# Kernel optimization log

Measured on AMD Instinct MI355X. Metric: run time of the kernel, lower is better.

## Reference

```python
import jax, jax.numpy as jnp
from jax import lax
import numpy as np

SEQ, FEAT, VOCAB = 59, 64, 578
B, U = 4096, 1024


def setup_inputs() -> dict:
    key = jax.random.key(0)
    ks = jax.random.split(key, 6)
    x = jax.random.normal(ks[0], (B, SEQ, FEAT), dtype=jnp.float32)
    # Keras LSTMCell params: kernel [feat, 4U], recurrent_kernel [U, 4U], bias [4U]
    kernel = jax.random.normal(ks[1], (FEAT, 4 * U), dtype=jnp.float32) * 0.05
    rec_kernel = jax.random.normal(ks[2], (U, 4 * U), dtype=jnp.float32) * 0.05
    bias = jnp.zeros((4 * U,), dtype=jnp.float32)
    w2 = jax.random.normal(ks[3], (U, VOCAB), dtype=jnp.float32) * 0.05
    b2 = jnp.zeros((VOCAB,), dtype=jnp.float32)
    return {"x": x, "kernel": kernel, "rec_kernel": rec_kernel, "bias": bias, "w2": w2, "b2": b2}


def reference(x, kernel, rec_kernel, bias, w2, b2):
    batch = x.shape[0]
    units = rec_kernel.shape[0]
    xs = jnp.transpose(x, (1, 0, 2))  # [SEQ, B, FEAT]
    h0 = jnp.zeros((batch, units), dtype=x.dtype)
    c0 = jnp.zeros((batch, units), dtype=x.dtype)

    def step(carry, xt):
        h, c = carry
        z = xt @ kernel + h @ rec_kernel + bias  # [B, 4U]
        i, f, g, o = jnp.split(z, 4, axis=-1)    # Keras gate order i,f,c,o
        i = jax.nn.sigmoid(i)
        f = jax.nn.sigmoid(f)
        g = jnp.tanh(g)
        o = jax.nn.sigmoid(o)
        c_new = f * c + i * g
        h_new = o * jnp.tanh(c_new)
        return (h_new, c_new), None

    (h_last, _), _ = lax.scan(step, (h0, c0), xs)
    probs = jax.nn.softmax(h_last @ w2 + b2, axis=-1)  # dense2 softmax on last hidden
    # original: stack single prediction -> [1,B,V], transpose [1,0,2] -> [B,1,V]
    return probs[:, None, :]
```

## Files before the change

kernel.cpp:

```cpp
#include <hip/hip_runtime.h>

#define SEQ    59
#define FEAT   64
#define VOCAB  578
#define BATCH  4096
#define UNITS  1024
#define KLSTM  1088
#define NPAD   640

typedef __bf16 bf16x8 __attribute__((ext_vector_type(8)));
typedef __bf16 bf16x4 __attribute__((ext_vector_type(4)));
typedef float  floatx4 __attribute__((ext_vector_type(4)));

typedef const __attribute__((address_space(1))) char gas_char;
typedef __attribute__((address_space(3))) char las_char;

__device__ __forceinline__ float sigmoid_f(float x) { return 1.f / (1.f + __expf(-x)); }
__device__ __forceinline__ float tanh_f(float x) { float e = __expf(2.f * x); return 1.f - 2.f / (e + 1.f); }


__global__ void convert_x_kernel(const float* __restrict__ x, __bf16* __restrict__ xbf) {
    int i = blockIdx.x * 256 + threadIdx.x;
    const int total = BATCH * SEQ * FEAT / 4;
    if (i >= total) return;
    float4 v = ((const float4*)x)[i];
    bf16x4 o;
    o.x = (__bf16)v.x; o.y = (__bf16)v.y; o.z = (__bf16)v.z; o.w = (__bf16)v.w;
    ((bf16x4*)xbf)[i] = o;
}

__global__ void convert_weights_kernel(const float* __restrict__ kern,
                                       const float* __restrict__ reck,
                                       __bf16* __restrict__ Wtp) {
    int idx = blockIdx.x * 256 + threadIdx.x;
    if (idx >= 4096 * KLSTM) return;
    int np = idx / KLSTM;
    int k  = idx - np * KLSTM;
    int ublk = np >> 7;
    int g    = (np >> 5) & 3;
    int j    = np & 31;
    int n    = g * 1024 + ublk * 32 + j;
    float v = (k < FEAT) ? kern[(size_t)k * 4096 + n]
                         : reck[(size_t)(k - FEAT) * 4096 + n];
    Wtp[idx] = (__bf16)v;
}

__global__ void convert_w2_kernel(const float* __restrict__ w2, __bf16* __restrict__ Wt2p) {
    int idx = blockIdx.x * 256 + threadIdx.x;
    if (idx >= NPAD * 1024) return;
    int n = idx >> 10;
    int k = idx & 1023;
    float v = (n < VOCAB) ? w2[(size_t)k * VOCAB + n] : 0.f;
    Wt2p[idx] = (__bf16)v;
}

__global__ void __launch_bounds__(256, 2) lstm_step_kernel(
    const __bf16* __restrict__ xbf,
    const __bf16* __restrict__ Wtp,
    const float*  __restrict__ bias,
    const __bf16* __restrict__ hin,
    __bf16*       __restrict__ hout,
    float*        __restrict__ cstate,
    int t)
{
    __shared__ __bf16 As[128 * 64];
    __shared__ __bf16 Bs[2][128 * 64];

    const int tid  = threadIdx.x;
    const int wid  = tid >> 6;
    const int lane = tid & 63;
    const int ln   = lane & 15;
    const int lk   = lane >> 4;
    const int wm   = wid >> 1;
    const int wn   = wid & 1;
    const int rb   = blockIdx.x;
    const int yb   = blockIdx.y;

    floatx4 acc[2][4][4];
#pragma unroll
    for (int p = 0; p < 2; ++p)
#pragma unroll
        for (int m = 0; m < 4; ++m)
#pragma unroll
            for (int g = 0; g < 4; ++g)
                acc[p][m][g] = (floatx4){0.f, 0.f, 0.f, 0.f};

    int s_row[4], s_kgd[4];
#pragma unroll
    for (int q = 0; q < 4; ++q) {
        int flat = q * 256 + tid;
        int row  = flat >> 3;
        s_row[q] = row;
        s_kgd[q] = (flat & 7) ^ (row & 7);
    }

    for (int kt = 0; kt < 17; ++kt) {
        __syncthreads();
#pragma unroll
        for (int q = 0; q < 4; ++q) {
            const int row = s_row[q], kgd = s_kgd[q];
            const __bf16* gp;
            if (kt == 0)
                gp = xbf + (size_t)(rb * 128 + row) * (SEQ * FEAT) + t * FEAT + kgd * 8;
            else
                gp = hin + ((size_t)(rb * 128 + row) << 10) + (kt - 1) * 64 + kgd * 8;
            __builtin_amdgcn_global_load_lds((gas_char*)gp,
                (las_char*)(As + (size_t)(q * 256 + (wid << 6)) * 8), 16, 0, 0);
        }
#pragma unroll
        for (int p = 0; p < 2; ++p) {
#pragma unroll
            for (int q = 0; q < 4; ++q) {
                const int n = s_row[q], kgd = s_kgd[q];
                const __bf16* gp = Wtp + (size_t)(yb * 256 + p * 128 + n) * KLSTM + kt * 64 + kgd * 8;
                __builtin_amdgcn_global_load_lds((gas_char*)gp,
                    (las_char*)(Bs[p] + (size_t)(q * 256 + (wid << 6)) * 8), 16, 0, 0);
            }
        }
        __syncthreads();
#pragma unroll
        for (int kk = 0; kk < 2; ++kk) {
            const int kg = kk * 4 + lk;
            bf16x8 a[4], b0[4], b1[4];
#pragma unroll
            for (int m = 0; m < 4; ++m) {
                int row  = wm * 64 + m * 16 + ln;
                int ccol = (kg ^ (row & 7)) * 8;
                a[m] = *(const bf16x8*)(As + row * 64 + ccol);
            }
#pragma unroll
            for (int g = 0; g < 4; ++g) {
                int n    = g * 32 + wn * 16 + ln;
                int ccol = (kg ^ (n & 7)) * 8;
                b0[g] = *(const bf16x8*)(Bs[0] + n * 64 + ccol);
                b1[g] = *(const bf16x8*)(Bs[1] + n * 64 + ccol);
            }
#pragma unroll
            for (int m = 0; m < 4; ++m)
#pragma unroll
                for (int g = 0; g < 4; ++g) {
                    acc[0][m][g] = __builtin_amdgcn_mfma_f32_16x16x32_bf16(a[m], b0[g], acc[0][m][g], 0, 0, 0);
                    acc[1][m][g] = __builtin_amdgcn_mfma_f32_16x16x32_bf16(a[m], b1[g], acc[1][m][g], 0, 0, 0);
                }
        }
    }

#pragma unroll
    for (int p = 0; p < 2; ++p) {
        const int u  = (yb * 2 + p) * 32 + wn * 16 + ln;
        const float bi  = bias[u];
        const float bfv = bias[UNITS + u];
        const float bg  = bias[2 * UNITS + u];
        const float bo  = bias[3 * UNITS + u];
#pragma unroll
        for (int m = 0; m < 4; ++m) {
            const int row0 = rb * 128 + wm * 64 + m * 16 + lk * 4;
#pragma unroll
            for (int r = 0; r < 4; ++r) {
                const size_t idx = ((size_t)(row0 + r) << 10) + u;
                float ig = sigmoid_f(acc[p][m][0][r] + bi);
                float fg = sigmoid_f(acc[p][m][1][r] + bfv);
                float gg = tanh_f(acc[p][m][2][r] + bg);
                float og = sigmoid_f(acc[p][m][3][r] + bo);
                float cn = fg * cstate[idx] + ig * gg;
                cstate[idx] = cn;
                hout[idx] = (__bf16)(og * tanh_f(cn));
            }
        }
    }
}

__global__ void __launch_bounds__(256) dense_kernel(
    const __bf16* __restrict__ hin,
    const __bf16* __restrict__ Wt2p,
    float*        __restrict__ logits)
{
    __shared__ __bf16 As[128 * 64];
    __shared__ __bf16 Bs[128 * 64];

    const int tid  = threadIdx.x;
    const int wid  = tid >> 6;
    const int lane = tid & 63;
    const int ln   = lane & 15;
    const int lk   = lane >> 4;
    const int wm   = wid >> 1;
    const int wn   = wid & 1;
    const int rb   = blockIdx.x;
    const int nb   = blockIdx.y;

    floatx4 acc[4][4];
#pragma unroll
    for (int m = 0; m < 4; ++m)
#pragma unroll
        for (int g = 0; g < 4; ++g)
            acc[m][g] = (floatx4){0.f, 0.f, 0.f, 0.f};

    int s_row[4], s_kgd[4];
#pragma unroll
    for (int q = 0; q < 4; ++q) {
        int flat = q * 256 + tid;
        int row  = flat >> 3;
        s_row[q] = row;
        s_kgd[q] = (flat & 7) ^ (row & 7);
    }

    for (int kt = 0; kt < 16; ++kt) {
        __syncthreads();
#pragma unroll
        for (int q = 0; q < 4; ++q) {
            const int row = s_row[q], kgd = s_kgd[q];
            const __bf16* gp = hin + ((size_t)(rb * 128 + row) << 10) + kt * 64 + kgd * 8;
            __builtin_amdgcn_global_load_lds((gas_char*)gp,
                (las_char*)(As + (size_t)(q * 256 + (wid << 6)) * 8), 16, 0, 0);
        }
#pragma unroll
        for (int q = 0; q < 4; ++q) {
            const int n = s_row[q], kgd = s_kgd[q];
            const __bf16* gp = Wt2p + ((size_t)(nb * 128 + n) << 10) + kt * 64 + kgd * 8;
            __builtin_amdgcn_global_load_lds((gas_char*)gp,
                (las_char*)(Bs + (size_t)(q * 256 + (wid << 6)) * 8), 16, 0, 0);
        }
        __syncthreads();
#pragma unroll
        for (int kk = 0; kk < 2; ++kk) {
            const int kg = kk * 4 + lk;
            bf16x8 a[4], b[4];
#pragma unroll
            for (int m = 0; m < 4; ++m) {
                int row  = wm * 64 + m * 16 + ln;
                int ccol = (kg ^ (row & 7)) * 8;
                a[m] = *(const bf16x8*)(As + row * 64 + ccol);
            }
#pragma unroll
            for (int g = 0; g < 4; ++g) {
                int n    = g * 32 + wn * 16 + ln;
                int ccol = (kg ^ (n & 7)) * 8;
                b[g] = *(const bf16x8*)(Bs + n * 64 + ccol);
            }
#pragma unroll
            for (int m = 0; m < 4; ++m)
#pragma unroll
                for (int g = 0; g < 4; ++g)
                    acc[m][g] = __builtin_amdgcn_mfma_f32_16x16x32_bf16(a[m], b[g], acc[m][g], 0, 0, 0);
        }
    }

#pragma unroll
    for (int m = 0; m < 4; ++m) {
        const int row0 = rb * 128 + wm * 64 + m * 16 + lk * 4;
#pragma unroll
        for (int g = 0; g < 4; ++g) {
            const int n = nb * 128 + g * 32 + wn * 16 + ln;
#pragma unroll
            for (int r = 0; r < 4; ++r)
                logits[(size_t)(row0 + r) * NPAD + n] = acc[m][g][r];
        }
    }
}

__global__ void __launch_bounds__(256) softmax_kernel(
    const float* __restrict__ logits,
    const float* __restrict__ b2,
    float* __restrict__ out)
{
    const int row = blockIdx.x;
    const int tid = threadIdx.x;
    __shared__ float red[8];

    float z[3];
    float lmax = -1e30f;
#pragma unroll
    for (int j = 0; j < 3; ++j) {
        int col = tid + j * 256;
        if (col < VOCAB) {
            z[j] = logits[(size_t)row * NPAD + col] + b2[col];
            lmax = fmaxf(lmax, z[j]);
        } else z[j] = -1e30f;
    }
    for (int off = 32; off > 0; off >>= 1) lmax = fmaxf(lmax, __shfl_xor(lmax, off));
    if ((tid & 63) == 0) red[tid >> 6] = lmax;
    __syncthreads();
    lmax = fmaxf(fmaxf(red[0], red[1]), fmaxf(red[2], red[3]));
    __syncthreads();

    float lsum = 0.f;
#pragma unroll
    for (int j = 0; j < 3; ++j) {
        int col = tid + j * 256;
        if (col < VOCAB) { z[j] = __expf(z[j] - lmax); lsum += z[j]; }
    }
    for (int off = 32; off > 0; off >>= 1) lsum += __shfl_xor(lsum, off);
    if ((tid & 63) == 0) red[tid >> 6] = lsum;
    __syncthreads();
    lsum = red[0] + red[1] + red[2] + red[3];
    float inv = 1.f / lsum;
#pragma unroll
    for (int j = 0; j < 3; ++j) {
        int col = tid + j * 256;
        if (col < VOCAB) out[(size_t)row * VOCAB + col] = z[j] * inv;
    }
}

extern "C" void kernel_launch(void* const* d_in, const int* in_sizes, int n_in,
                              void* d_out, int out_size, void* d_ws, size_t ws_size,
                              hipStream_t stream)
{
    const float* x    = (const float*)d_in[0];
    const float* kern = (const float*)d_in[1];
    const float* reck = (const float*)d_in[2];
    const float* bias = (const float*)d_in[3];
    const float* w2   = (const float*)d_in[4];
    const float* b2   = (const float*)d_in[5];
    float* out = (float*)d_out;

    char* ws = (char*)d_ws;
    size_t off = 0;
    auto alloc = [&](size_t bytes) {
        char* p = ws + off;
        off += (bytes + 255) & ~(size_t)255;
        return p;
    };
    __bf16* Wtp    = (__bf16*)alloc((size_t)4096 * KLSTM * 2);
    __bf16* Wt2p   = (__bf16*)alloc((size_t)NPAD * 1024 * 2);
    __bf16* xbf    = (__bf16*)alloc((size_t)BATCH * SEQ * FEAT * 2);
    __bf16* h0     = (__bf16*)alloc((size_t)BATCH * UNITS * 2);
    __bf16* h1     = (__bf16*)alloc((size_t)BATCH * UNITS * 2);
    float*  cst    = (float*)alloc((size_t)BATCH * UNITS * 4);
    float*  logits = (float*)alloc((size_t)BATCH * NPAD * 4);
    if (off > ws_size) return;

    (void)hipMemsetAsync(h0, 0, (size_t)BATCH * UNITS * 2, stream);
    (void)hipMemsetAsync(cst, 0, (size_t)BATCH * UNITS * 4, stream);

    convert_x_kernel<<<(BATCH * SEQ * FEAT / 4 + 255) / 256, 256, 0, stream>>>(x, xbf);
    convert_weights_kernel<<<(4096 * KLSTM + 255) / 256, 256, 0, stream>>>(kern, reck, Wtp);
    convert_w2_kernel<<<(NPAD * 1024 + 255) / 256, 256, 0, stream>>>(w2, Wt2p);

    __bf16* hin = h0; __bf16* hout = h1;
    for (int t = 0; t < SEQ; ++t) {
        lstm_step_kernel<<<dim3(32, 16), 256, 0, stream>>>(xbf, Wtp, bias, hin, hout, cst, t);
        __bf16* tmp = hin; hin = hout; hout = tmp;
    }

    dense_kernel<<<dim3(32, 5), 256, 0, stream>>>(hin, Wt2p, logits);
    softmax_kernel<<<BATCH, 256, 0, stream>>>(logits, b2, out);
}
```

Baseline: 2.578 ms.

## Load LSTM GEMM operands directly from global memory into registers, dropping LDS staging

Removes the shared-memory tiles and the two barriers per k-step in the LSTM step kernel. Each wave now loads its A (x or h) and B (weight) fragments straight from global memory into registers and feeds them to MFMA. This saves LDS traffic and synchronisation, but loses the sharing of tiles across waves. Each weight and hidden row is now fetched by several waves through the caches, and the per-lane 16-byte loads along rows are poorly coalesced.

```diff
diff --git a/kernel.cpp b/kernel.cpp
--- a/kernel.cpp
+++ b/kernel.cpp
@@ -63,9 +63,6 @@
     float*        __restrict__ cstate,
     int t)
 {
-    __shared__ __bf16 As[128 * 64];
-    __shared__ __bf16 Bs[2][128 * 64];
-
     const int tid  = threadIdx.x;
     const int wid  = tid >> 6;
     const int lane = tid & 63;
@@ -85,62 +82,66 @@
             for (int g = 0; g < 4; ++g)
                 acc[p][m][g] = (floatx4){0.f, 0.f, 0.f, 0.f};
 
-    int s_row[4], s_kgd[4];
-#pragma unroll
-    for (int q = 0; q < 4; ++q) {
-        int flat = q * 256 + tid;
-        int row  = flat >> 3;
-        s_row[q] = row;
-        s_kgd[q] = (flat & 7) ^ (row & 7);
-    }
-
-    for (int kt = 0; kt < 17; ++kt) {
-        __syncthreads();
-#pragma unroll
-        for (int q = 0; q < 4; ++q) {
-            const int row = s_row[q], kgd = s_kgd[q];
-            const __bf16* gp;
-            if (kt == 0)
-                gp = xbf + (size_t)(rb * 128 + row) * (SEQ * FEAT) + t * FEAT + kgd * 8;
-            else
-                gp = hin + ((size_t)(rb * 128 + row) << 10) + (kt - 1) * 64 + kgd * 8;
-            __builtin_amdgcn_global_load_lds((gas_char*)gp,
-                (las_char*)(As + (size_t)(q * 256 + (wid << 6)) * 8), 16, 0, 0);
-        }
-#pragma unroll
-        for (int p = 0; p < 2; ++p) {
-#pragma unroll
-            for (int q = 0; q < 4; ++q) {
-                const int n = s_row[q], kgd = s_kgd[q];
-                const __bf16* gp = Wtp + (size_t)(yb * 256 + p * 128 + n) * KLSTM + kt * 64 + kgd * 8;
-                __builtin_amdgcn_global_load_lds((gas_char*)gp,
-                    (las_char*)(Bs[p] + (size_t)(q * 256 + (wid << 6)) * 8), 16, 0, 0);
+    const __bf16* aBase[4];
+#pragma unroll
+    for (int m = 0; m < 4; ++m) {
+        const int row = rb * 128 + wm * 64 + m * 16 + ln;
+        aBase[m] = hin + ((size_t)row << 10);
+    }
+    const __bf16* bBase[2][4];
+#pragma unroll
+    for (int p = 0; p < 2; ++p)
+#pragma unroll
+        for (int g = 0; g < 4; ++g) {
+            const int n = yb * 256 + p * 128 + g * 32 + wn * 16 + ln;
+            bBase[p][g] = Wtp + (size_t)n * KLSTM;
+        }
+
+#pragma unroll
+    for (int kk = 0; kk < 2; ++kk) {
+        const int kg = kk * 4 + lk;
+        bf16x8 a[4], b[2][4];
+#pragma unroll
+        for (int m = 0; m < 4; ++m) {
+            const int row = rb * 128 + wm * 64 + m * 16 + ln;
+            a[m] = *(const bf16x8*)(xbf + (size_t)row * (SEQ * FEAT) + t * FEAT + kg * 8);
+        }
+#pragma unroll
+        for (int p = 0; p < 2; ++p)
+#pragma unroll
+            for (int g = 0; g < 4; ++g)
+                b[p][g] = *(const bf16x8*)(bBase[p][g] + kg * 8);
+#pragma unroll
+        for (int m = 0; m < 4; ++m)
+#pragma unroll
+            for (int g = 0; g < 4; ++g) {
+                acc[0][m][g] = __builtin_amdgcn_mfma_f32_16x16x32_bf16(a[m], b[0][g], acc[0][m][g], 0, 0, 0);
+                acc[1][m][g] = __builtin_amdgcn_mfma_f32_16x16x32_bf16(a[m], b[1][g], acc[1][m][g], 0, 0, 0);
             }
-        }
-        __syncthreads();
+    }
+
+#pragma unroll 2
+    for (int kt = 1; kt < 17; ++kt) {
+        const int ka = (kt - 1) * 64;
+        const int kb = kt * 64;
 #pragma unroll
         for (int kk = 0; kk < 2; ++kk) {
             const int kg = kk * 4 + lk;
-            bf16x8 a[4], b0[4], b1[4];
-#pragma unroll
-            for (int m = 0; m < 4; ++m) {
-                int row  = wm * 64 + m * 16 + ln;
-                int ccol = (kg ^ (row & 7)) * 8;
-                a[m] = *(const bf16x8*)(As + row * 64 + ccol);
-            }
-#pragma unroll
-            for (int g = 0; g < 4; ++g) {
-                int n    = g * 32 + wn * 16 + ln;
-                int ccol = (kg ^ (n & 7)) * 8;
-                b0[g] = *(const bf16x8*)(Bs[0] + n * 64 + ccol);
-                b1[g] = *(const bf16x8*)(Bs[1] + n * 64 + ccol);
-            }
+            bf16x8 a[4], b[2][4];
 #pragma unroll
             for (int m = 0; m < 4; ++m)
+                a[m] = *(const bf16x8*)(aBase[m] + ka + kg * 8);
+#pragma unroll
+            for (int p = 0; p < 2; ++p)
+#pragma unroll
+                for (int g = 0; g < 4; ++g)
+                    b[p][g] = *(const bf16x8*)(bBase[p][g] + kb + kg * 8);
+#pragma unroll
+            for (int m = 0; m < 4; ++m)
 #pragma unroll
                 for (int g = 0; g < 4; ++g) {
-                    acc[0][m][g] = __builtin_amdgcn_mfma_f32_16x16x32_bf16(a[m], b0[g], acc[0][m][g], 0, 0, 0);
-                    acc[1][m][g] = __builtin_amdgcn_mfma_f32_16x16x32_bf16(a[m], b1[g], acc[1][m][g], 0, 0, 0);
+                    acc[0][m][g] = __builtin_amdgcn_mfma_f32_16x16x32_bf16(a[m], b[0][g], acc[0][m][g], 0, 0, 0);
+                    acc[1][m][g] = __builtin_amdgcn_mfma_f32_16x16x32_bf16(a[m], b[1][g], acc[1][m][g], 0, 0, 0);
                 }
         }
     }
```

Result: slower. 6.309 ms (+144.8%).

## Fuse LSTM timesteps into one persistent kernel with per-row-block flag sync

Applied to the files above, without the earlier changes.

Replaces 59 per-timestep kernel launches with a single persistent kernel of 512 blocks that loops over time. Blocks that share a batch row block synchronize through atomic done counters, spinning until all 16 column blocks have finished the previous step. This removes launch overhead and the full-grid barrier implied by each launch, letting independent row blocks run ahead. It relies on all 512 blocks being co-resident (2 per CU), uses glc/slc-style loads for h to avoid stale cache data, and adds spin-wait cost.

```diff
diff --git a/kernel.cpp b/kernel.cpp
--- a/kernel.cpp
+++ b/kernel.cpp
@@ -54,14 +54,14 @@
     Wt2p[idx] = (__bf16)v;
 }
 
-__global__ void __launch_bounds__(256, 2) lstm_step_kernel(
+__global__ void __launch_bounds__(256, 2) lstm_seq_kernel(
     const __bf16* __restrict__ xbf,
     const __bf16* __restrict__ Wtp,
     const float*  __restrict__ bias,
-    const __bf16* __restrict__ hin,
-    __bf16*       __restrict__ hout,
-    float*        __restrict__ cstate,
-    int t)
+    __bf16* __restrict__ hbuf0,
+    __bf16* __restrict__ hbuf1,
+    float*  __restrict__ cstate,
+    int*    __restrict__ done)
 {
     __shared__ __bf16 As[128 * 64];
     __shared__ __bf16 Bs[2][128 * 64];
@@ -73,17 +73,9 @@
     const int lk   = lane >> 4;
     const int wm   = wid >> 1;
     const int wn   = wid & 1;
-    const int rb   = blockIdx.x;
-    const int yb   = blockIdx.y;
-
-    floatx4 acc[2][4][4];
-#pragma unroll
-    for (int p = 0; p < 2; ++p)
-#pragma unroll
-        for (int m = 0; m < 4; ++m)
-#pragma unroll
-            for (int g = 0; g < 4; ++g)
-                acc[p][m][g] = (floatx4){0.f, 0.f, 0.f, 0.f};
+    const int bid  = blockIdx.x;
+    const int rb   = bid >> 4;
+    const int yb   = bid & 15;
 
     int s_row[4], s_kgd[4];
 #pragma unroll
@@ -94,79 +86,116 @@
         s_kgd[q] = (flat & 7) ^ (row & 7);
     }
 
-    for (int kt = 0; kt < 17; ++kt) {
+    const int u0 = (yb * 2 + 0) * 32 + wn * 16 + ln;
+    const int u1 = (yb * 2 + 1) * 32 + wn * 16 + ln;
+
+#pragma unroll 1
+    for (int t = 0; t < SEQ; ++t) {
+        const __bf16* hin  = (t & 1) ? hbuf1 : hbuf0;
+        __bf16*       hout = (t & 1) ? hbuf0 : hbuf1;
+
+        if (t > 0) {
+            if (tid == 0) {
+                const int* fp = &done[(rb << 6) + (t - 1)];
+                while (__hip_atomic_load(fp, __ATOMIC_RELAXED, __HIP_MEMORY_SCOPE_AGENT) < 16)
+                    __builtin_amdgcn_s_sleep(2);
+            }
+            __syncthreads();
+        }
+
+        floatx4 acc[2][4][4];
+#pragma unroll
+        for (int p = 0; p < 2; ++p)
+#pragma unroll
+            for (int m = 0; m < 4; ++m)
+#pragma unroll
+                for (int g = 0; g < 4; ++g)
+                    acc[p][m][g] = (floatx4){0.f, 0.f, 0.f, 0.f};
+
+        for (int kt = 0; kt < 17; ++kt) {
+            __syncthreads();
+#pragma unroll
+            for (int q = 0; q < 4; ++q) {
+                const int row = s_row[q], kgd = s_kgd[q];
+                if (kt == 0) {
+                    const __bf16* gp = xbf + (size_t)(rb * 128 + row) * (SEQ * FEAT) + t * FEAT + kgd * 8;
+                    __builtin_amdgcn_global_load_lds((gas_char*)gp,
+                        (las_char*)(As + (size_t)(q * 256 + (wid << 6)) * 8), 16, 0, 0);
+                } else {
+                    const __bf16* gp = hin + ((size_t)(rb * 128 + row) << 10) + (kt - 1) * 64 + kgd * 8;
+                    __builtin_amdgcn_global_load_lds((gas_char*)gp,
+                        (las_char*)(As + (size_t)(q * 256 + (wid << 6)) * 8), 16, 0, 17);
+                }
+            }
+#pragma unroll
+            for (int p = 0; p < 2; ++p) {
+#pragma unroll
+                for (int q = 0; q < 4; ++q) {
+                    const int n = s_row[q], kgd = s_kgd[q];
+                    const __bf16* gp = Wtp + (size_t)(yb * 256 + p * 128 + n) * KLSTM + kt * 64 + kgd * 8;
+                    __builtin_amdgcn_global_load_lds((gas_char*)gp,
+                        (las_char*)(Bs[p] + (size_t)(q * 256 + (wid << 6)) * 8), 16, 0, 0);
+                }
+            }
+            __syncthreads();
+#pragma unroll
+            for (int kk = 0; kk < 2; ++kk) {
+                const int kg = kk * 4 + lk;
+                bf16x8 a[4], b0[4], b1[4];
+#pragma unroll
+                for (int m = 0; m < 4; ++m) {
+                    int row  = wm * 64 + m * 16 + ln;
+                    int ccol = (kg ^ (row & 7)) * 8;
+                    a[m] = *(const bf16x8*)(As + row * 64 + ccol);
+                }
+#pragma unroll
+                for (int g = 0; g < 4; ++g) {
+                    int n    = g * 32 + wn * 16 + ln;
+                    int ccol = (kg ^ (n & 7)) * 8;
+                    b0[g] = *(const bf16x8*)(Bs[0] + n * 64 + ccol);
+                    b1[g] = *(const bf16x8*)(Bs[1] + n * 64 + ccol);
+                }
+#pragma unroll
+                for (int m = 0; m < 4; ++m)
+#pragma unroll
+                    for (int g = 0; g < 4; ++g) {
+                        acc[0][m][g] = __builtin_amdgcn_mfma_f32_16x16x32_bf16(a[m], b0[g], acc[0][m][g], 0, 0, 0);
+                        acc[1][m][g] = __builtin_amdgcn_mfma_f32_16x16x32_bf16(a[m], b1[g], acc[1][m][g], 0, 0, 0);
+                    }
+            }
+        }
+
+#pragma unroll
+        for (int p = 0; p < 2; ++p) {
+            const int u = p ? u1 : u0;
+            const float bi  = bias[u];
+            const float bfv = bias[UNITS + u];
+            const float bg  = bias[2 * UNITS + u];
+            const float bo  = bias[3 * UNITS + u];
+#pragma unroll
+            for (int m = 0; m < 4; ++m) {
+                const int row0 = rb * 128 + wm * 64 + m * 16 + lk * 4;
+#pragma unroll
+                for (int r = 0; r < 4; ++r) {
+                    const size_t idx = ((size_t)(row0 + r) << 10) + u;
+                    float ig = sigmoid_f(acc[p][m][0][r] + bi);
+                    float fg = sigmoid_f(acc[p][m][1][r] + bfv);
+                    float gg = tanh_f(acc[p][m][2][r] + bg);
+                    float og = sigmoid_f(acc[p][m][3][r] + bo);
+                    float cold = __hip_atomic_load(&cstate[idx], __ATOMIC_RELAXED, __HIP_MEMORY_SCOPE_WORKGROUP);
+                    float cn = fg * cold + ig * gg;
+                    cstate[idx] = cn;
+                    unsigned short hb = __builtin_bit_cast(unsigned short, (__bf16)(og * tanh_f(cn)));
+                    __hip_atomic_store((unsigned short*)hout + idx, hb,
+                                       __ATOMIC_RELAXED, __HIP_MEMORY_SCOPE_AGENT);
+                }
+            }
+        }
+
         __syncthreads();
-#pragma unroll
-        for (int q = 0; q < 4; ++q) {
-            const int row = s_row[q], kgd = s_kgd[q];
-            const __bf16* gp;
-            if (kt == 0)
-                gp = xbf + (size_t)(rb * 128 + row) * (SEQ * FEAT) + t * FEAT + kgd * 8;
-            else
-                gp = hin + ((size_t)(rb * 128 + row) << 10) + (kt - 1) * 64 + kgd * 8;
-            __builtin_amdgcn_global_load_lds((gas_char*)gp,
-                (las_char*)(As + (size_t)(q * 256 + (wid << 6)) * 8), 16, 0, 0);
-        }
-#pragma unroll
-        for (int p = 0; p < 2; ++p) {
-#pragma unroll
-            for (int q = 0; q < 4; ++q) {
-                const int n = s_row[q], kgd = s_kgd[q];
-                const __bf16* gp = Wtp + (size_t)(yb * 256 + p * 128 + n) * KLSTM + kt * 64 + kgd * 8;
-                __builtin_amdgcn_global_load_lds((gas_char*)gp,
-                    (las_char*)(Bs[p] + (size_t)(q * 256 + (wid << 6)) * 8), 16, 0, 0);
-            }
-        }
-        __syncthreads();
-#pragma unroll
-        for (int kk = 0; kk < 2; ++kk) {
-            const int kg = kk * 4 + lk;
-            bf16x8 a[4], b0[4], b1[4];
-#pragma unroll
-            for (int m = 0; m < 4; ++m) {
-                int row  = wm * 64 + m * 16 + ln;
-                int ccol = (kg ^ (row & 7)) * 8;
-                a[m] = *(const bf16x8*)(As + row * 64 + ccol);
-            }
-#pragma unroll
-            for (int g = 0; g < 4; ++g) {
-                int n    = g * 32 + wn * 16 + ln;
-                int ccol = (kg ^ (n & 7)) * 8;
-                b0[g] = *(const bf16x8*)(Bs[0] + n * 64 + ccol);
-                b1[g] = *(const bf16x8*)(Bs[1] + n * 64 + ccol);
-            }
-#pragma unroll
-            for (int m = 0; m < 4; ++m)
-#pragma unroll
-                for (int g = 0; g < 4; ++g) {
-                    acc[0][m][g] = __builtin_amdgcn_mfma_f32_16x16x32_bf16(a[m], b0[g], acc[0][m][g], 0, 0, 0);
-                    acc[1][m][g] = __builtin_amdgcn_mfma_f32_16x16x32_bf16(a[m], b1[g], acc[1][m][g], 0, 0, 0);
-                }
-        }
-    }
-
-#pragma unroll
-    for (int p = 0; p < 2; ++p) {
-        const int u  = (yb * 2 + p) * 32 + wn * 16 + ln;
-        const float bi  = bias[u];
-        const float bfv = bias[UNITS + u];
-        const float bg  = bias[2 * UNITS + u];
-        const float bo  = bias[3 * UNITS + u];
-#pragma unroll
-        for (int m = 0; m < 4; ++m) {
-            const int row0 = rb * 128 + wm * 64 + m * 16 + lk * 4;
-#pragma unroll
-            for (int r = 0; r < 4; ++r) {
-                const size_t idx = ((size_t)(row0 + r) << 10) + u;
-                float ig = sigmoid_f(acc[p][m][0][r] + bi);
-                float fg = sigmoid_f(acc[p][m][1][r] + bfv);
-                float gg = tanh_f(acc[p][m][2][r] + bg);
-                float og = sigmoid_f(acc[p][m][3][r] + bo);
-                float cn = fg * cstate[idx] + ig * gg;
-                cstate[idx] = cn;
-                hout[idx] = (__bf16)(og * tanh_f(cn));
-            }
-        }
+        if (tid == 0)
+            __hip_atomic_fetch_add(&done[(rb << 6) + t], 1,
+                                   __ATOMIC_RELAXED, __HIP_MEMORY_SCOPE_AGENT);
     }
 }
 
@@ -327,21 +356,19 @@
     __bf16* h1     = (__bf16*)alloc((size_t)BATCH * UNITS * 2);
     float*  cst    = (float*)alloc((size_t)BATCH * UNITS * 4);
     float*  logits = (float*)alloc((size_t)BATCH * NPAD * 4);
+    int*    done   = (int*)alloc((size_t)32 * 64 * 4);
     if (off > ws_size) return;
 
     (void)hipMemsetAsync(h0, 0, (size_t)BATCH * UNITS * 2, stream);
     (void)hipMemsetAsync(cst, 0, (size_t)BATCH * UNITS * 4, stream);
+    (void)hipMemsetAsync(done, 0, (size_t)32 * 64 * 4, stream);
 
     convert_x_kernel<<<(BATCH * SEQ * FEAT / 4 + 255) / 256, 256, 0, stream>>>(x, xbf);
     convert_weights_kernel<<<(4096 * KLSTM + 255) / 256, 256, 0, stream>>>(kern, reck, Wtp);
     convert_w2_kernel<<<(NPAD * 1024 + 255) / 256, 256, 0, stream>>>(w2, Wt2p);
 
-    __bf16* hin = h0; __bf16* hout = h1;
-    for (int t = 0; t < SEQ; ++t) {
-        lstm_step_kernel<<<dim3(32, 16), 256, 0, stream>>>(xbf, Wtp, bias, hin, hout, cst, t);
-        __bf16* tmp = hin; hin = hout; hout = tmp;
-    }
-
-    dense_kernel<<<dim3(32, 5), 256, 0, stream>>>(hin, Wt2p, logits);
+    lstm_seq_kernel<<<512, 256, 0, stream>>>(xbf, Wtp, bias, h0, h1, cst, done);
+
+    dense_kernel<<<dim3(32, 5), 256, 0, stream>>>(h1, Wt2p, logits);
     softmax_kernel<<<BATCH, 256, 0, stream>>>(logits, b2, out);
 }
```

New measurement: 3.589 ms. 39.2% more time.

## Warp-specialize LSTM step into producer/consumer waves with double-buffered LDS

Applied to the files above, without the earlier changes.

Splits each LSTM step block into four loader waves that stream A/B tiles into two LDS buffers and four MFMA waves that consume them, synchronized by shared-memory ready/done counters with spin-waits. Each block now processes two consecutive N-tiles, giving 256 blocks of 512 threads, which overlaps global loads with compute across k-steps and tiles. This costs 96KB of dynamic LDS per block, likely limiting occupancy, and adds spin-wait overhead plus a risk of deadlock or ordering errors in the flag protocol.

```diff
diff --git a/kernel.cpp b/kernel.cpp
--- a/kernel.cpp
+++ b/kernel.cpp
@@ -8,6 +8,9 @@
 #define KLSTM  1088
 #define NPAD   640
 
+#define CWAVES 4
+#define PWAVES 4
+
 typedef __bf16 bf16x8 __attribute__((ext_vector_type(8)));
 typedef __bf16 bf16x4 __attribute__((ext_vector_type(4)));
 typedef float  floatx4 __attribute__((ext_vector_type(4)));
@@ -17,6 +20,11 @@
 
 __device__ __forceinline__ float sigmoid_f(float x) { return 1.f / (1.f + __expf(-x)); }
 __device__ __forceinline__ float tanh_f(float x) { float e = __expf(2.f * x); return 1.f - 2.f / (e + 1.f); }
+
+__device__ __forceinline__ void spin_ge(int* f, int target) {
+    while (__hip_atomic_load(f, __ATOMIC_ACQUIRE, __HIP_MEMORY_SCOPE_WORKGROUP) < target)
+        __builtin_amdgcn_s_sleep(1);
+}
 
 
 __global__ void convert_x_kernel(const float* __restrict__ x, __bf16* __restrict__ xbf) {
@@ -54,7 +62,7 @@
     Wt2p[idx] = (__bf16)v;
 }
 
-__global__ void __launch_bounds__(256, 2) lstm_step_kernel(
+__global__ void __launch_bounds__(512, 2) lstm_step_kernel(
     const __bf16* __restrict__ xbf,
     const __bf16* __restrict__ Wtp,
     const float*  __restrict__ bias,
@@ -63,108 +71,146 @@
     float*        __restrict__ cstate,
     int t)
 {
-    __shared__ __bf16 As[128 * 64];
-    __shared__ __bf16 Bs[2][128 * 64];
+    extern __shared__ __bf16 smem[];
+    __bf16* As = smem;
+    __bf16* Bs = smem + 2 * 8192;
+    __shared__ int rdy[2];
+    __shared__ int dn[2];
 
     const int tid  = threadIdx.x;
     const int wid  = tid >> 6;
     const int lane = tid & 63;
-    const int ln   = lane & 15;
-    const int lk   = lane >> 4;
-    const int wm   = wid >> 1;
-    const int wn   = wid & 1;
-    const int rb   = blockIdx.x;
-    const int yb   = blockIdx.y;
-
-    floatx4 acc[2][4][4];
-#pragma unroll
-    for (int p = 0; p < 2; ++p)
-#pragma unroll
-        for (int m = 0; m < 4; ++m)
-#pragma unroll
-            for (int g = 0; g < 4; ++g)
-                acc[p][m][g] = (floatx4){0.f, 0.f, 0.f, 0.f};
-
-    int s_row[4], s_kgd[4];
-#pragma unroll
-    for (int q = 0; q < 4; ++q) {
-        int flat = q * 256 + tid;
-        int row  = flat >> 3;
-        s_row[q] = row;
-        s_kgd[q] = (flat & 7) ^ (row & 7);
-    }
-
-    for (int kt = 0; kt < 17; ++kt) {
-        __syncthreads();
+    const int bid  = blockIdx.x;
+    const int Yp   = bid & 7;
+    const int rb   = bid >> 3;
+
+    if (tid < 2) { rdy[tid] = 0; dn[tid] = 0; }
+    __syncthreads();
+
+    if (wid >= CWAVES) {
+        const int ptid = tid - CWAVES * 64;
+        const int pwid = wid - CWAVES;
+        int s_row[4], s_kgd[4];
 #pragma unroll
         for (int q = 0; q < 4; ++q) {
-            const int row = s_row[q], kgd = s_kgd[q];
-            const __bf16* gp;
-            if (kt == 0)
-                gp = xbf + (size_t)(rb * 128 + row) * (SEQ * FEAT) + t * FEAT + kgd * 8;
-            else
-                gp = hin + ((size_t)(rb * 128 + row) << 10) + (kt - 1) * 64 + kgd * 8;
-            __builtin_amdgcn_global_load_lds((gas_char*)gp,
-                (las_char*)(As + (size_t)(q * 256 + (wid << 6)) * 8), 16, 0, 0);
-        }
-#pragma unroll
-        for (int p = 0; p < 2; ++p) {
+            int flat = q * 256 + ptid;
+            int row  = flat >> 3;
+            s_row[q] = row;
+            s_kgd[q] = (flat & 7) ^ (row & 7);
+        }
+#pragma unroll 1
+        for (int phase = 0; phase < 34; ++phase) {
+            const int b   = phase & 1;
+            const int r   = phase >> 1;
+            const int sub = (phase >= 17) ? 1 : 0;
+            const int kt  = phase - sub * 17;
+            const int Y   = Yp * 2 + sub;
+            if (phase >= 2) spin_ge(&dn[b], CWAVES * r);
+            __bf16* Ad = As + b * 8192;
+            __bf16* Bd = Bs + b * 2 * 8192;
 #pragma unroll
             for (int q = 0; q < 4; ++q) {
-                const int n = s_row[q], kgd = s_kgd[q];
-                const __bf16* gp = Wtp + (size_t)(yb * 256 + p * 128 + n) * KLSTM + kt * 64 + kgd * 8;
+                const int row = s_row[q], kgd = s_kgd[q];
+                const __bf16* gp;
+                if (kt == 0)
+                    gp = xbf + (size_t)(rb * 128 + row) * (SEQ * FEAT) + t * FEAT + kgd * 8;
+                else
+                    gp = hin + ((size_t)(rb * 128 + row) << 10) + (kt - 1) * 64 + kgd * 8;
                 __builtin_amdgcn_global_load_lds((gas_char*)gp,
-                    (las_char*)(Bs[p] + (size_t)(q * 256 + (wid << 6)) * 8), 16, 0, 0);
-            }
-        }
-        __syncthreads();
-#pragma unroll
-        for (int kk = 0; kk < 2; ++kk) {
-            const int kg = kk * 4 + lk;
-            bf16x8 a[4], b0[4], b1[4];
-#pragma unroll
-            for (int m = 0; m < 4; ++m) {
-                int row  = wm * 64 + m * 16 + ln;
-                int ccol = (kg ^ (row & 7)) * 8;
-                a[m] = *(const bf16x8*)(As + row * 64 + ccol);
-            }
-#pragma unroll
-            for (int g = 0; g < 4; ++g) {
-                int n    = g * 32 + wn * 16 + ln;
-                int ccol = (kg ^ (n & 7)) * 8;
-                b0[g] = *(const bf16x8*)(Bs[0] + n * 64 + ccol);
-                b1[g] = *(const bf16x8*)(Bs[1] + n * 64 + ccol);
-            }
-#pragma unroll
-            for (int m = 0; m < 4; ++m)
-#pragma unroll
-                for (int g = 0; g < 4; ++g) {
-                    acc[0][m][g] = __builtin_amdgcn_mfma_f32_16x16x32_bf16(a[m], b0[g], acc[0][m][g], 0, 0, 0);
-                    acc[1][m][g] = __builtin_amdgcn_mfma_f32_16x16x32_bf16(a[m], b1[g], acc[1][m][g], 0, 0, 0);
+                    (las_char*)(Ad + (size_t)(q * 256 + (pwid << 6)) * 8), 16, 0, 0);
+            }
+#pragma unroll
+            for (int p = 0; p < 2; ++p) {
+#pragma unroll
+                for (int q = 0; q < 4; ++q) {
+                    const int n = s_row[q], kgd = s_kgd[q];
+                    const __bf16* gp = Wtp + (size_t)(Y * 256 + p * 128 + n) * KLSTM + kt * 64 + kgd * 8;
+                    __builtin_amdgcn_global_load_lds((gas_char*)gp,
+                        (las_char*)(Bd + p * 8192 + (size_t)(q * 256 + (pwid << 6)) * 8), 16, 0, 0);
                 }
-        }
-    }
-
-#pragma unroll
-    for (int p = 0; p < 2; ++p) {
-        const int u  = (yb * 2 + p) * 32 + wn * 16 + ln;
-        const float bi  = bias[u];
-        const float bfv = bias[UNITS + u];
-        const float bg  = bias[2 * UNITS + u];
-        const float bo  = bias[3 * UNITS + u];
-#pragma unroll
-        for (int m = 0; m < 4; ++m) {
-            const int row0 = rb * 128 + wm * 64 + m * 16 + lk * 4;
-#pragma unroll
-            for (int r = 0; r < 4; ++r) {
-                const size_t idx = ((size_t)(row0 + r) << 10) + u;
-                float ig = sigmoid_f(acc[p][m][0][r] + bi);
-                float fg = sigmoid_f(acc[p][m][1][r] + bfv);
-                float gg = tanh_f(acc[p][m][2][r] + bg);
-                float og = sigmoid_f(acc[p][m][3][r] + bo);
-                float cn = fg * cstate[idx] + ig * gg;
-                cstate[idx] = cn;
-                hout[idx] = (__bf16)(og * tanh_f(cn));
+            }
+            __builtin_amdgcn_s_waitcnt(0x0F70);
+            if (lane == 0)
+                __hip_atomic_fetch_add(&rdy[b], 1, __ATOMIC_RELEASE, __HIP_MEMORY_SCOPE_WORKGROUP);
+        }
+    } else {
+        const int ln = lane & 15;
+        const int lk = lane >> 4;
+        const int wm = wid >> 1;
+        const int wn = wid & 1;
+
+#pragma unroll 1
+        for (int sub = 0; sub < 2; ++sub) {
+            const int Y = Yp * 2 + sub;
+            floatx4 acc[2][4][4];
+#pragma unroll
+            for (int p = 0; p < 2; ++p)
+#pragma unroll
+                for (int m = 0; m < 4; ++m)
+#pragma unroll
+                    for (int g = 0; g < 4; ++g)
+                        acc[p][m][g] = (floatx4){0.f, 0.f, 0.f, 0.f};
+
+#pragma unroll 1
+            for (int kt = 0; kt < 17; ++kt) {
+                const int phase = sub * 17 + kt;
+                const int b = phase & 1;
+                const int r = phase >> 1;
+                spin_ge(&rdy[b], PWAVES * (r + 1));
+                const __bf16* Ab  = As + b * 8192;
+                const __bf16* Bb0 = Bs + b * 2 * 8192;
+                const __bf16* Bb1 = Bb0 + 8192;
+#pragma unroll
+                for (int kk = 0; kk < 2; ++kk) {
+                    const int kg = kk * 4 + lk;
+                    bf16x8 a[4], b0[4], b1[4];
+#pragma unroll
+                    for (int m = 0; m < 4; ++m) {
+                        int row  = wm * 64 + m * 16 + ln;
+                        int ccol = (kg ^ (row & 7)) * 8;
+                        a[m] = *(const bf16x8*)(Ab + row * 64 + ccol);
+                    }
+#pragma unroll
+                    for (int g = 0; g < 4; ++g) {
+                        int n    = g * 32 + wn * 16 + ln;
+                        int ccol = (kg ^ (n & 7)) * 8;
+                        b0[g] = *(const bf16x8*)(Bb0 + n * 64 + ccol);
+                        b1[g] = *(const bf16x8*)(Bb1 + n * 64 + ccol);
+                    }
+#pragma unroll
+                    for (int m = 0; m < 4; ++m)
+#pragma unroll
+                        for (int g = 0; g < 4; ++g) {
+                            acc[0][m][g] = __builtin_amdgcn_mfma_f32_16x16x32_bf16(a[m], b0[g], acc[0][m][g], 0, 0, 0);
+                            acc[1][m][g] = __builtin_amdgcn_mfma_f32_16x16x32_bf16(a[m], b1[g], acc[1][m][g], 0, 0, 0);
+                        }
+                }
+                if (lane == 0)
+                    __hip_atomic_fetch_add(&dn[b], 1, __ATOMIC_RELEASE, __HIP_MEMORY_SCOPE_WORKGROUP);
+            }
+
+#pragma unroll
+            for (int p = 0; p < 2; ++p) {
+                const int u  = (Y * 2 + p) * 32 + wn * 16 + ln;
+                const float bi  = bias[u];
+                const float bfv = bias[UNITS + u];
+                const float bg  = bias[2 * UNITS + u];
+                const float bo  = bias[3 * UNITS + u];
+#pragma unroll
+                for (int m = 0; m < 4; ++m) {
+                    const int row0 = rb * 128 + wm * 64 + m * 16 + lk * 4;
+#pragma unroll
+                    for (int rr = 0; rr < 4; ++rr) {
+                        const size_t idx = ((size_t)(row0 + rr) << 10) + u;
+                        float ig = sigmoid_f(acc[p][m][0][rr] + bi);
+                        float fg = sigmoid_f(acc[p][m][1][rr] + bfv);
+                        float gg = tanh_f(acc[p][m][2][rr] + bg);
+                        float og = sigmoid_f(acc[p][m][3][rr] + bo);
+                        float cn = fg * cstate[idx] + ig * gg;
+                        cstate[idx] = cn;
+                        hout[idx] = (__bf16)(og * tanh_f(cn));
+                    }
+                }
             }
         }
     }
@@ -329,6 +375,9 @@
     float*  logits = (float*)alloc((size_t)BATCH * NPAD * 4);
     if (off > ws_size) return;
 
+    (void)hipFuncSetAttribute((const void*)lstm_step_kernel,
+                              hipFuncAttributeMaxDynamicSharedMemorySize, 96 * 1024);
+
     (void)hipMemsetAsync(h0, 0, (size_t)BATCH * UNITS * 2, stream);
     (void)hipMemsetAsync(cst, 0, (size_t)BATCH * UNITS * 4, stream);
 
@@ -338,7 +387,7 @@
 
     __bf16* hin = h0; __bf16* hout = h1;
     for (int t = 0; t < SEQ; ++t) {
-        lstm_step_kernel<<<dim3(32, 16), 256, 0, stream>>>(xbf, Wtp, bias, hin, hout, cst, t);
+        lstm_step_kernel<<<256, 512, 96 * 1024, stream>>>(xbf, Wtp, bias, hin, hout, cst, t);
         __bf16* tmp = hin; hin = hout; hout = tmp;
     }
 
```

Result: slower. 3.365 ms (+30.5%).
